# Kernel optimization log

Hardware: AMD Instinct MI355X
Metric: run time of the kernel (lower is better)

The kernel has to match this reference:

```python
import jax, jax.numpy as jnp
import numpy as np

N = 100000
DIM = 128
N_EDGES = 3200000
EPS = 1e-5


def setup_inputs() -> dict:
    key = jax.random.key(0)
    k1, k2, k3, k4, k5, k6 = jax.random.split(key, 6)
    x = jax.random.normal(k1, (N, DIM), dtype=jnp.float32)
    edge_row = jnp.sort(jax.random.randint(k2, (N_EDGES,), 0, N, dtype=jnp.int64))
    edge_col = jax.random.randint(k3, (N_EDGES,), 0, N, dtype=jnp.int64)
    edge_val = jax.random.uniform(k4, (N_EDGES,), dtype=jnp.float32)
    gamma = jnp.ones((DIM,), dtype=jnp.float32)
    beta = jnp.zeros((DIM,), dtype=jnp.float32)
    return {"x": x, "edge_row": edge_row, "edge_col": edge_col,
            "edge_val": edge_val, "gamma": gamma, "beta": beta}


def _layernorm(h, gamma, beta):
    mu = jnp.mean(h, axis=-1, keepdims=True)
    var = jnp.mean(jnp.square(h - mu), axis=-1, keepdims=True)
    return (h - mu) * jax.lax.rsqrt(var + EPS) * gamma + beta


def reference(x, edge_row, edge_col, edge_val, gamma, beta):
    # sparse adj @ x  ==  segment-sum of val * x[src] into dst rows
    msgs = edge_val[:, None] * x[edge_col]            # [E, DIM]
    h = jax.ops.segment_sum(msgs, edge_row, num_segments=N)  # [N, DIM]
    return _layernorm(h + x, gamma, beta)
```

## Files before the change

### kernel.cpp

```cpp
#include <hip/hip_runtime.h>
#include <hip/hip_fp16.h>

#define DIM 128
#define EPS 1e-5f
#define WPB 4
#define UF  4

__global__ void prep_kernel(const float4* __restrict__ x4,
                            __half2* __restrict__ xh2,
                            const int* __restrict__ edge_row,
                            int* __restrict__ row_ptr,
                            int n4, int n_nodes, int n_edges)
{
    int i = blockIdx.x * blockDim.x + threadIdx.x;
    if (i < n4) {
        float4 v = x4[i];
        xh2[2 * i]     = __float22half2_rn(make_float2(v.x, v.y));
        xh2[2 * i + 1] = __float22half2_rn(make_float2(v.z, v.w));
    }
    if (i < n_edges) {
        int cur  = edge_row[i];
        int prev = (i == 0) ? -1 : edge_row[i - 1];
        for (int r = prev + 1; r <= cur; ++r) row_ptr[r] = i;
        if (i == n_edges - 1) {
            for (int r = cur + 1; r <= n_nodes; ++r) row_ptr[r] = n_edges;
        }
    }
}

__global__ __launch_bounds__(WPB * 64)
void gnn_fused_kernel(const uint4* __restrict__ xh16,
                      const int*   __restrict__ row_ptr,
                      const int*   __restrict__ edge_col,
                      const float* __restrict__ edge_val,
                      const float* __restrict__ gamma,
                      const float* __restrict__ beta,
                      float*       __restrict__ out,
                      int n_nodes, int n_edges)
{
    const int wave = threadIdx.x >> 6;
    const int lane = threadIdx.x & 63;
    const int q    = lane >> 4;
    const int sub  = lane & 15;
    const int node = blockIdx.x * WPB + wave;
    if (node >= n_nodes) return;

    const int start = row_ptr[node];
    const int end   = row_ptr[node + 1];
    const unsigned len = (unsigned)(end - start);

    float acc[8];
#pragma unroll
    for (int k = 0; k < 8; ++k) acc[k] = 0.f;

    const int ebase = start & ~3;
    for (int e0 = ebase; e0 < end; e0 += 4 * UF) {
        int   c[UF];
        float w[UF];
#pragma unroll
        for (int u = 0; u < UF; ++u) {
            int ei = e0 + 4 * u + q;
            int eb = min(ei, n_edges - 1);
            bool in = (unsigned)(ei - start) < len;
            int   cc = edge_col[eb];
            float ww = edge_val[eb];
            c[u] = in ? cc : 0;
            w[u] = in ? ww : 0.f;
        }
        uint4 v[UF];
#pragma unroll
        for (int u = 0; u < UF; ++u)
            v[u] = xh16[c[u] * (DIM / 8) + sub];
#pragma unroll
        for (int u = 0; u < UF; ++u) {
            const __half2* hp = (const __half2*)&v[u];
#pragma unroll
            for (int j = 0; j < 4; ++j) {
                float2 f = __half22float2(hp[j]);
                acc[2 * j]     = fmaf(w[u], f.x, acc[2 * j]);
                acc[2 * j + 1] = fmaf(w[u], f.y, acc[2 * j + 1]);
            }
        }
    }

#pragma unroll
    for (int k = 0; k < 8; ++k) {
        acc[k] += __shfl_xor(acc[k], 16, 64);
        acc[k] += __shfl_xor(acc[k], 32, 64);
    }

    uint4 xv = xh16[node * (DIM / 8) + sub];
    const __half2* xp = (const __half2*)&xv;
    float h[8];
#pragma unroll
    for (int j = 0; j < 4; ++j) {
        float2 f = __half22float2(xp[j]);
        h[2 * j]     = acc[2 * j]     + f.x;
        h[2 * j + 1] = acc[2 * j + 1] + f.y;
    }

    float s = 0.f, sq = 0.f;
#pragma unroll
    for (int k = 0; k < 8; ++k) { s += h[k]; sq += h[k] * h[k]; }
#pragma unroll
    for (int off = 1; off <= 8; off <<= 1) {
        s  += __shfl_xor(s,  off, 64);
        sq += __shfl_xor(sq, off, 64);
    }
    const float mean = s * (1.0f / (float)DIM);
    const float var  = sq * (1.0f / (float)DIM) - mean * mean;
    const float rs   = rsqrtf(var + EPS);

    float hx = (q < 2) ? ((q == 0) ? h[0] : h[2]) : ((q == 2) ? h[4] : h[6]);
    float hy = (q < 2) ? ((q == 0) ? h[1] : h[3]) : ((q == 2) ? h[5] : h[7]);
    const int didx = sub * 4 + q;
    const float2 g = ((const float2*)gamma)[didx];
    const float2 b = ((const float2*)beta)[didx];
    float2 o;
    o.x = (hx - mean) * rs * g.x + b.x;
    o.y = (hy - mean) * rs * g.y + b.y;
    ((float2*)out)[node * (DIM / 2) + didx] = o;
}

extern "C" void kernel_launch(void* const* d_in, const int* in_sizes, int n_in,
                              void* d_out, int out_size, void* d_ws, size_t ws_size,
                              hipStream_t stream)
{
    const float* x        = (const float*)d_in[0];
    const int*   edge_row = (const int*)  d_in[1];
    const int*   edge_col = (const int*)  d_in[2];
    const float* edge_val = (const float*)d_in[3];
    const float* gamma    = (const float*)d_in[4];
    const float* beta     = (const float*)d_in[5];
    float*       out      = (float*)d_out;

    const int n_nodes = in_sizes[0] / DIM;
    const int n_edges = in_sizes[1];
    const int n_elem  = in_sizes[0];
    const int n4      = n_elem / 4;

    __half2* xh2     = (__half2*)d_ws;
    int*     row_ptr = (int*)((char*)d_ws + (size_t)n_elem * sizeof(__half));

    int prep_threads = (n4 > n_edges) ? n4 : n_edges;
    prep_kernel<<<(prep_threads + 255) / 256, 256, 0, stream>>>(
        (const float4*)x, xh2, edge_row, row_ptr, n4, n_nodes, n_edges);

    const int blocks = (n_nodes + WPB - 1) / WPB;
    gnn_fused_kernel<<<blocks, WPB * 64, 0, stream>>>(
        (const uint4*)d_ws, row_ptr, edge_col, edge_val, gamma, beta, out,
        n_nodes, n_edges);
}
```

Measured before the change: 235.7 us.

## Vectorize edge index loads per quarter-wave and double the unroll factor

Each quarter-wave now handles eight contiguous edges, read as two 128-bit nontemporal vector loads for both column indices and values, instead of strided scalar loads. The unroll factor rises from 4 to 8, so 32 edges are gathered per wave iteration with more feature-row loads in flight. The output write also becomes a nontemporal store. Costs are higher register use, which may lower occupancy, and extra masked-out work for low-degree rows. It also relies on the edge count being a multiple of four to keep the clamped vector loads aligned and correct.

```diff
diff --git a/kernel.cpp b/kernel.cpp
--- a/kernel.cpp
+++ b/kernel.cpp
@@ -4,7 +4,11 @@
 #define DIM 128
 #define EPS 1e-5f
 #define WPB 4
-#define UF  4
+#define UF  8
+
+typedef int   vint4   __attribute__((ext_vector_type(4)));
+typedef float vfloat4 __attribute__((ext_vector_type(4)));
+typedef float vfloat2 __attribute__((ext_vector_type(2)));
 
 __global__ void prep_kernel(const float4* __restrict__ x4,
                             __half2* __restrict__ xh2,
@@ -54,32 +58,38 @@
     for (int k = 0; k < 8; ++k) acc[k] = 0.f;
 
     const int ebase = start & ~3;
+    const int emax  = n_edges - 4;
     for (int e0 = ebase; e0 < end; e0 += 4 * UF) {
-        int   c[UF];
-        float w[UF];
+        const int b0  = e0 + q * UF;
+        const int b0c = min(b0, emax);
+        const int b1c = min(b0 + 4, emax);
+        vint4   ca = __builtin_nontemporal_load((const vint4*)  (edge_col + b0c));
+        vint4   cb = __builtin_nontemporal_load((const vint4*)  (edge_col + b1c));
+        vfloat4 wa = __builtin_nontemporal_load((const vfloat4*)(edge_val + b0c));
+        vfloat4 wb = __builtin_nontemporal_load((const vfloat4*)(edge_val + b1c));
+
+        int   c[UF] = {ca.x, ca.y, ca.z, ca.w, cb.x, cb.y, cb.z, cb.w};
+        float w[UF] = {wa.x, wa.y, wa.z, wa.w, wb.x, wb.y, wb.z, wb.w};
+
+        const int off = b0 - start;
 #pragma unroll
         for (int u = 0; u < UF; ++u) {
-            int ei = e0 + 4 * u + q;
-            int eb = min(ei, n_edges - 1);
-            bool in = (unsigned)(ei - start) < len;
-            int   cc = edge_col[eb];
-            float ww = edge_val[eb];
-            c[u] = in ? cc : 0;
-            w[u] = in ? ww : 0.f;
+            bool in = (unsigned)(off + u) < len;
+            c[u] = in ? c[u] : 0;
+            w[u] = in ? w[u] : 0.f;
         }
+
         uint4 v[UF];
 #pragma unroll
         for (int u = 0; u < UF; ++u)
             v[u] = xh16[c[u] * (DIM / 8) + sub];
+
 #pragma unroll
         for (int u = 0; u < UF; ++u) {
-            const __half2* hp = (const __half2*)&v[u];
+            const __half* hp = (const __half*)&v[u];
 #pragma unroll
-            for (int j = 0; j < 4; ++j) {
-                float2 f = __half22float2(hp[j]);
-                acc[2 * j]     = fmaf(w[u], f.x, acc[2 * j]);
-                acc[2 * j + 1] = fmaf(w[u], f.y, acc[2 * j + 1]);
-            }
+            for (int j = 0; j < 8; ++j)
+                acc[j] = fmaf(w[u], __half2float(hp[j]), acc[j]);
         }
     }
 
@@ -90,14 +100,10 @@
     }
 
     uint4 xv = xh16[node * (DIM / 8) + sub];
-    const __half2* xp = (const __half2*)&xv;
+    const __half* xp = (const __half*)&xv;
     float h[8];
 #pragma unroll
-    for (int j = 0; j < 4; ++j) {
-        float2 f = __half22float2(xp[j]);
-        h[2 * j]     = acc[2 * j]     + f.x;
-        h[2 * j + 1] = acc[2 * j + 1] + f.y;
-    }
+    for (int j = 0; j < 8; ++j) h[j] = acc[j] + __half2float(xp[j]);
 
     float s = 0.f, sq = 0.f;
 #pragma unroll
@@ -116,10 +122,10 @@
     const int didx = sub * 4 + q;
     const float2 g = ((const float2*)gamma)[didx];
     const float2 b = ((const float2*)beta)[didx];
-    float2 o;
+    vfloat2 o;
     o.x = (hx - mean) * rs * g.x + b.x;
     o.y = (hy - mean) * rs * g.y + b.y;
-    ((float2*)out)[node * (DIM / 2) + didx] = o;
+    __builtin_nontemporal_store(o, (vfloat2*)out + node * (DIM / 2) + didx);
 }
 
 extern "C" void kernel_launch(void* const* d_in, const int* in_sizes, int n_in,
```

Result: slower. 243.6 us (+3.3%).
